# Performance work log

Measured on AMD Instinct MI355X. Metric: run time of the kernel, lower is better.

Reference implementation:

```python
import jax, jax.numpy as jnp
import numpy as np

B, L, ENC_IN, C_OUT = 4, 2048, 64, 64
D_MODEL, N_HEADS, D_FF, E_LAYERS = 1024, 16, 4096, 4
CA_K = 5  # ChannelAttention1D kernel: int(|log2(1024)+1|/2)=5 (odd)


def _layer_norm(x, w, b, eps=1e-5):
    m = x.mean(-1, keepdims=True)
    v = ((x - m) ** 2).mean(-1, keepdims=True)
    return (x - m) * jax.lax.rsqrt(v + eps) * w + b


def _flow_attention(q, k, v):
    # q,k,v: [B, L, H, D] -> work in [B, H, L, D]
    q = jax.nn.sigmoid(jnp.swapaxes(q, 1, 2))
    k = jax.nn.sigmoid(jnp.swapaxes(k, 1, 2))
    v = jnp.swapaxes(v, 1, 2)
    eps = 1e-6
    Lq = q.shape[2]
    S = k.shape[2]
    nr = 1.0 / jnp.einsum('bhld,bhd->bhl', q + eps, k.sum(axis=2) + eps)
    nc = 1.0 / jnp.einsum('bhsd,bhd->bhs', k + eps, q.sum(axis=2) + eps)
    nrr = jnp.einsum('bhld,bhd->bhl', q + eps, (k * nc[..., None]).sum(axis=2) + eps)
    ncr = jnp.einsum('bhsd,bhd->bhs', k + eps, (q * nr[..., None]).sum(axis=2) + eps)
    nrr = jax.nn.sigmoid(nrr * (float(Lq) / float(S)))
    ncr = jax.nn.softmax(ncr, axis=-1) * S
    kv = jnp.einsum('bhsd,bhse->bhde', k, v * ncr[..., None])  # [B,H,D,Dv]
    out = jnp.einsum('bhld,bhde->bhle', q, kv) * nr[..., None] * nrr[..., None]
    return jnp.swapaxes(out, 1, 2)  # [B, L, H, Dv]


def _token_embed(x, w):
    # x: [B, L, Cin]; circular conv1d kernel=3, pad=1, no bias
    xt = jnp.swapaxes(x, 1, 2)  # [B, Cin, L]
    xt = jnp.concatenate([xt[..., -1:], xt, xt[..., :1]], axis=-1)
    y = jax.lax.conv_general_dilated(xt, w, (1,), 'VALID',
                                     dimension_numbers=('NCH', 'OIH', 'NCH'))
    return jnp.swapaxes(y, 1, 2)  # [B, L, d_model]


def _channel_att(x, w):
    # x: [B, L, C]; squeeze over L, conv over channel axis, sigmoid gate
    y = x.mean(axis=1, keepdims=True)  # [B, 1, C]
    pad = CA_K // 2
    yp = jnp.pad(y, ((0, 0), (0, 0), (pad, pad)))
    yc = jax.lax.conv_general_dilated(yp, w.reshape(1, 1, CA_K), (1,), 'VALID',
                                      dimension_numbers=('NCH', 'OIH', 'NCH'))
    return x * jax.nn.sigmoid(yc)


def _encoder_layer(x, Wq, bq, Wk, bk, Wv, bv, Wo, bo,
                   ln1w, ln1b, ln2w, ln2b, c1w, c1b, c2w, c2b):
    Bx, Lx, _ = x.shape
    q = (x @ Wq.T + bq).reshape(Bx, Lx, N_HEADS, -1)
    k = (x @ Wk.T + bk).reshape(Bx, Lx, N_HEADS, -1)
    v = (x @ Wv.T + bv).reshape(Bx, Lx, N_HEADS, -1)
    a = _flow_attention(q, k, v).reshape(Bx, Lx, -1)
    a = a @ Wo.T + bo
    x = _layer_norm(x + a, ln1w, ln1b)
    y = jax.nn.relu(jnp.einsum('bld,fd->blf', x, c1w) + c1b)  # conv1 k=1
    y = jnp.einsum('blf,df->bld', y, c2w) + c2b               # conv2 k=1
    return _layer_norm(x + y, ln2w, ln2b)


def setup_inputs() -> dict:
    key = jax.random.key(0)
    ks = jax.random.split(key, 16)
    s = 0.02
    E, D, F = E_LAYERS, D_MODEL, D_FF
    inp = {
        'x': jax.random.normal(ks[0], (B, L, ENC_IN), jnp.float32),
        'tok_conv_w': jax.random.normal(ks[1], (D, ENC_IN, 3), jnp.float32) * s,
        'Wq': jax.random.normal(ks[2], (E, D, D), jnp.float32) * s,
        'bq': jnp.zeros((E, D), jnp.float32),
        'Wk': jax.random.normal(ks[3], (E, D, D), jnp.float32) * s,
        'bk': jnp.zeros((E, D), jnp.float32),
        'Wv': jax.random.normal(ks[4], (E, D, D), jnp.float32) * s,
        'bv': jnp.zeros((E, D), jnp.float32),
        'Wo': jax.random.normal(ks[5], (E, D, D), jnp.float32) * s,
        'bo': jnp.zeros((E, D), jnp.float32),
        'conv1_w': jax.random.normal(ks[6], (E, F, D), jnp.float32) * s,
        'conv1_b': jnp.zeros((E, F), jnp.float32),
        'conv2_w': jax.random.normal(ks[7], (E, D, F), jnp.float32) * s,
        'conv2_b': jnp.zeros((E, D), jnp.float32),
        'ln1_w': jnp.ones((E, D), jnp.float32),
        'ln1_b': jnp.zeros((E, D), jnp.float32),
        'ln2_w': jnp.ones((E, D), jnp.float32),
        'ln2_b': jnp.zeros((E, D), jnp.float32),
        'ca_w': jax.random.normal(ks[8], (E, CA_K), jnp.float32) * 0.2,
        'lnf_w': jnp.ones((D,), jnp.float32),
        'lnf_b': jnp.zeros((D,), jnp.float32),
        'proj_w': jax.random.normal(ks[9], (C_OUT, D), jnp.float32) * s,
        'proj_b': jnp.zeros((C_OUT,), jnp.float32),
    }
    return inp


def reference(x, tok_conv_w, Wq, bq, Wk, bk, Wv, bv, Wo, bo,
              conv1_w, conv1_b, conv2_w, conv2_b,
              ln1_w, ln1_b, ln2_w, ln2_b, ca_w,
              lnf_w, lnf_b, proj_w, proj_b):
    h = _token_embed(x, tok_conv_w)  # dropout = identity (eval)
    for i in range(E_LAYERS):
        h = _encoder_layer(h, Wq[i], bq[i], Wk[i], bk[i], Wv[i], bv[i], Wo[i], bo[i],
                           ln1_w[i], ln1_b[i], ln2_w[i], ln2_b[i],
                           conv1_w[i], conv1_b[i], conv2_w[i], conv2_b[i])
        h = _channel_att(h, ca_w[i])
    # Encoder re-applies the last attention layer after the conv loop (faithful)
    i = E_LAYERS - 1
    h = _encoder_layer(h, Wq[i], bq[i], Wk[i], bk[i], Wv[i], bv[i], Wo[i], bo[i],
                       ln1_w[i], ln1_b[i], ln2_w[i], ln2_b[i],
                       conv1_w[i], conv1_b[i], conv2_w[i], conv2_b[i])
    h = _layer_norm(h, lnf_w, lnf_b)
    return h @ proj_w.T + proj_b
```

## Files before the change

### kernel.cpp

```cpp
#include <hip/hip_runtime.h>
#include <stdint.h>

#define L_SEQ 2048
#define DM 1024
#define NH 16
#define DFF 4096
#define NB 4
#define ROWS (NB * L_SEQ)

typedef __attribute__((ext_vector_type(8))) __bf16 bf16x8;
typedef __attribute__((ext_vector_type(4))) float f32x4;

__device__ __forceinline__ float bf2f(unsigned short u) {
  union { unsigned int i; float f; } x; x.i = ((unsigned int)u) << 16; return x.f;
}
__device__ __forceinline__ unsigned short f2bf(float f) {
  union { float f; unsigned int i; } x; x.f = f;
  unsigned int r = x.i + 0x7FFFu + ((x.i >> 16) & 1u);
  return (unsigned short)(r >> 16);
}

typedef __attribute__((address_space(3))) void lds_void;
typedef const __attribute__((address_space(1))) void gbl_void;

__device__ __forceinline__ void stage16(const void* g, void* ldsbase) {
  __builtin_amdgcn_global_load_lds((gbl_void*)g, (lds_void*)ldsbase, 16, 0, 0);
}

#define MFMA1(d, a, b) (d) = __builtin_amdgcn_mfma_f32_16x16x32_bf16((a), (b), (d), 0, 0, 0)

__global__ __launch_bounds__(256, 4)
void gemm_f(const unsigned short* __restrict__ A,
            const unsigned short* __restrict__ B,
            const float* __restrict__ bias,
            unsigned short* __restrict__ C16,
            float* __restrict__ C32,
            int K, int lda, int ldc, int n_limit, int act)
{
  __shared__ __attribute__((aligned(16))) unsigned short sm[16384];
  char* smb = (char*)sm;
  const int tid  = threadIdx.x;
  const int wave = tid >> 6, lane = tid & 63;
  const int l16 = lane & 15, quad = lane >> 4;
  const int lb = lane << 4;
  const int wm = wave >> 1, wn = wave & 1;

  const int bx = (int)blockIdx.x, by = (int)blockIdx.y;

  const unsigned short* Ab = A + (size_t)bx * 128 * lda;
  const unsigned short* Bb = B + (size_t)by * 128 * K;

  const int rb0 = ((wave >> 1) << 4) + l16;
  const int cb0 = ((wave & 1) << 5) + (quad << 3);

  f32x4 acc[4][4] = {};
  const int T = K >> 6;

  for (int t = 0; t < T; ++t) {
    const unsigned short* sa = Ab + (size_t)rb0 * lda + t * 64 + cb0;
    const unsigned short* sb = Bb + (size_t)rb0 * K   + t * 64 + cb0;
    char* da = smb + wave * 1024;
    char* db = smb + 16384 + wave * 1024;
#pragma unroll
    for (int j = 0; j < 4; ++j) {
      stage16(sa + (size_t)(j * 32) * lda, da + j * 4096);
      stage16(sb + (size_t)(j * 32) * K,   db + j * 4096);
    }
    __syncthreads();
#pragma unroll
    for (int ks = 0; ks < 2; ++ks) {
      bf16x8 af[4], bf[4];
#pragma unroll
      for (int i = 0; i < 4; ++i) {
        af[i] = *(const bf16x8*)(smb + ((((wm * 4 + i) * 2 + ks)) << 10) + lb);
        bf[i] = *(const bf16x8*)(smb + 16384 + ((((wn * 4 + i) * 2 + ks)) << 10) + lb);
      }
#pragma unroll
      for (int i = 0; i < 4; ++i)
#pragma unroll
        for (int j = 0; j < 4; ++j)
          MFMA1(acc[i][j], af[i], bf[j]);
    }
    __syncthreads();
  }

  const int row0 = bx * 128 + wm * 64 + quad * 4;
  const int col0 = by * 128 + wn * 64 + l16;
#pragma unroll
  for (int nj = 0; nj < 4; ++nj) {
    const int col = col0 + nj * 16;
    if (col >= n_limit) continue;
    const float bv = bias ? bias[col] : 0.0f;
    const bool sig = (act == 2) || (act == 3 && col < 2048);
#pragma unroll
    for (int mi = 0; mi < 4; ++mi) {
#pragma unroll
      for (int r = 0; r < 4; ++r) {
        const int row = row0 + mi * 16 + r;
        float v = acc[mi][nj][r] + bv;
        if (act == 1) v = fmaxf(v, 0.0f);
        else if (sig) v = 1.0f / (1.0f + __expf(-v));
        if (C32) C32[(size_t)row * ldc + col] = v;
        if (C16) C16[(size_t)row * ldc + col] = f2bf(v);
      }
    }
  }
}


__global__ __launch_bounds__(256)
void fa_sums(const unsigned short* __restrict__ Q, const unsigned short* __restrict__ K,
             int ld, float* __restrict__ ksp, float* __restrict__ qsp)
{
  const int bh = blockIdx.x, chunk = blockIdx.y;
  const size_t base = ((size_t)(bh >> 4) * L_SEQ) * ld + (size_t)(bh & 15) * 64;
  const int t = threadIdx.x, lane = t & 63, wave = t >> 6;
  __shared__ float red[256];
  float ks = 0.f, qs = 0.f;
  const int l0 = chunk * 256 + wave * 64;
  for (int i = 0; i < 64; i++) {
    const size_t idx = base + (size_t)(l0 + i) * ld + lane;
    ks += bf2f(K[idx]);
    qs += bf2f(Q[idx]);
  }
  red[t] = ks; __syncthreads();
  if (t < 64) ksp[(bh * 8 + chunk) * 64 + t] = red[t] + red[t + 64] + red[t + 128] + red[t + 192];
  __syncthreads();
  red[t] = qs; __syncthreads();
  if (t < 64) qsp[(bh * 8 + chunk) * 64 + t] = red[t] + red[t + 64] + red[t + 128] + red[t + 192];
}

__global__ __launch_bounds__(256)
void fa_rows1(const unsigned short* __restrict__ Q, const unsigned short* __restrict__ K,
              int ld, const float* __restrict__ ksp, const float* __restrict__ qsp,
              float* __restrict__ nr, float* __restrict__ t1p, float* __restrict__ t2p)
{
  const int bh = blockIdx.x, chunk = blockIdx.y;
  const size_t base = ((size_t)(bh >> 4) * L_SEQ) * ld + (size_t)(bh & 15) * 64;
  const int t = threadIdx.x, lane = t & 63, wave = t >> 6;
  const float eps = 1e-6f;
  __shared__ float s_kse[64], s_qse[64], red[256];
  if (t < 64) {
    float s = 0.f;
    for (int j = 0; j < 8; j++) s += ksp[(bh * 8 + j) * 64 + t];
    s_kse[t] = s + eps;
  } else if (t < 128) {
    const int d = t - 64;
    float s = 0.f;
    for (int j = 0; j < 8; j++) s += qsp[(bh * 8 + j) * 64 + d];
    s_qse[d] = s + eps;
  }
  __syncthreads();
  const float kse = s_kse[lane], qse = s_qse[lane];
  float t1a = 0.f, t2a = 0.f;
  for (int i = 0; i < 32; i++) {
    const int l = chunk * 128 + wave + 4 * i;
    const size_t idx = base + (size_t)l * ld + lane;
    const float q = bf2f(Q[idx]), k = bf2f(K[idx]);
    float a = (q + eps) * kse;
    float c = (k + eps) * qse;
#pragma unroll
    for (int off = 32; off; off >>= 1) { a += __shfl_xor(a, off); c += __shfl_xor(c, off); }
    const float nrl = 1.f / a, ncl = 1.f / c;
    if (lane == 0) nr[bh * L_SEQ + l] = nrl;
    t1a += k * ncl;
    t2a += q * nrl;
  }
  red[t] = t1a; __syncthreads();
  if (t < 64) t1p[(bh * 16 + chunk) * 64 + t] = red[t] + red[t + 64] + red[t + 128] + red[t + 192];
  __syncthreads();
  red[t] = t2a; __syncthreads();
  if (t < 64) t2p[(bh * 16 + chunk) * 64 + t] = red[t] + red[t + 64] + red[t + 128] + red[t + 192];
}

__global__ __launch_bounds__(256)
void fa_rows2(const unsigned short* __restrict__ Q, const unsigned short* __restrict__ K,
              int ld, const float* __restrict__ t1p, const float* __restrict__ t2p,
              float* __restrict__ nr, float* __restrict__ sc)
{
  const int bh = blockIdx.x, chunk = blockIdx.y;
  const size_t base = ((size_t)(bh >> 4) * L_SEQ) * ld + (size_t)(bh & 15) * 64;
  const int t = threadIdx.x, lane = t & 63, wave = t >> 6;
  const float eps = 1e-6f;
  __shared__ float s_t1e[64], s_t2e[64];
  if (t < 64) {
    float s = 0.f;
    for (int j = 0; j < 16; j++) s += t1p[(bh * 16 + j) * 64 + t];
    s_t1e[t] = s + eps;
  } else if (t < 128) {
    const int d = t - 64;
    float s = 0.f;
    for (int j = 0; j < 16; j++) s += t2p[(bh * 16 + j) * 64 + d];
    s_t2e[d] = s + eps;
  }
  __syncthreads();
  const float t1e = s_t1e[lane], t2e = s_t2e[lane];
  for (int i = 0; i < 32; i++) {
    const int l = chunk * 128 + wave + 4 * i;
    const size_t idx = base + (size_t)l * ld + lane;
    const float q = bf2f(Q[idx]), k = bf2f(K[idx]);
    float a = (q + eps) * t1e;
    float c = (k + eps) * t2e;
#pragma unroll
    for (int off = 32; off; off >>= 1) { a += __shfl_xor(a, off); c += __shfl_xor(c, off); }
    if (lane == 0) {
      nr[bh * L_SEQ + l] *= 1.f / (1.f + __expf(-a));
      sc[bh * L_SEQ + l] = c;
    }
  }
}

__global__ __launch_bounds__(256)
void fa_softmax(float* __restrict__ sc, float* __restrict__ kv)
{
  const int bh = blockIdx.x, t = threadIdx.x;
  __shared__ float red[256];
  float4* kvz = (float4*)(kv + bh * 64 * 64);
  for (int j = 0; j < 4; j++) kvz[t + 256 * j] = make_float4(0.f, 0.f, 0.f, 0.f);

  float* row = sc + bh * L_SEQ;
  float m = -3.4e38f;
  for (int l = t; l < L_SEQ; l += 256) m = fmaxf(m, row[l]);
  red[t] = m; __syncthreads();
  for (int s = 128; s > 0; s >>= 1) { if (t < s) red[t] = fmaxf(red[t], red[t + s]); __syncthreads(); }
  const float mx = red[0];
  __syncthreads();
  float ps = 0.f;
  float pv[8];
#pragma unroll
  for (int j = 0; j < 8; j++) {
    const int l = t + 256 * j;
    pv[j] = __expf(row[l] - mx);
    ps += pv[j];
  }
  red[t] = ps; __syncthreads();
  for (int s = 128; s > 0; s >>= 1) { if (t < s) red[t] += red[t + s]; __syncthreads(); }
  const float scale = (float)L_SEQ / red[0];
#pragma unroll
  for (int j = 0; j < 8; j++) row[t + 256 * j] = pv[j] * scale;
}

__global__ __launch_bounds__(256)
void fa_kv(const unsigned short* __restrict__ K, const unsigned short* __restrict__ V,
           int ld, const float* __restrict__ sc, float* __restrict__ kv)
{
  const int bh = blockIdx.x, chunk = blockIdx.y;
  const size_t base = ((size_t)(bh >> 4) * L_SEQ) * ld + (size_t)(bh & 15) * 64;
  const int t = threadIdx.x, lane = t & 63, wave = t >> 6;
  const int l16 = lane & 15, quad = lane >> 4;
  __shared__ __attribute__((aligned(16))) unsigned short s_kT[64 * 72];
  __shared__ __attribute__((aligned(16))) unsigned short s_vT[64 * 72];

  f32x4 acc5[4] = {};
  for (int sub = 0; sub < 2; sub++) {
    const int l0 = chunk * 128 + sub * 64;
#pragma unroll
    for (int it = 0; it < 4; it++) {
      const int task = it * 256 + t;
      const int l = task >> 4;
      const int g = task & 15;
      const size_t gidx = base + (size_t)(l0 + l) * ld + g * 4;
      const ushort4 k4 = *(const ushort4*)(K + gidx);
      const ushort4 v4 = *(const ushort4*)(V + gidx);
      const float wgt = sc[bh * L_SEQ + l0 + l];
      s_kT[(g * 4 + 0) * 72 + l] = k4.x;
      s_kT[(g * 4 + 1) * 72 + l] = k4.y;
      s_kT[(g * 4 + 2) * 72 + l] = k4.z;
      s_kT[(g * 4 + 3) * 72 + l] = k4.w;
      s_vT[(g * 4 + 0) * 72 + l] = f2bf(bf2f(v4.x) * wgt);
      s_vT[(g * 4 + 1) * 72 + l] = f2bf(bf2f(v4.y) * wgt);
      s_vT[(g * 4 + 2) * 72 + l] = f2bf(bf2f(v4.z) * wgt);
      s_vT[(g * 4 + 3) * 72 + l] = f2bf(bf2f(v4.w) * wgt);
    }
    __syncthreads();
#pragma unroll
    for (int ks = 0; ks < 2; ks++) {
      const bf16x8 af = *(const bf16x8*)&s_kT[(wave * 16 + l16) * 72 + ks * 32 + quad * 8];
#pragma unroll
      for (int et = 0; et < 4; et++) {
        const bf16x8 bf = *(const bf16x8*)&s_vT[(et * 16 + l16) * 72 + ks * 32 + quad * 8];
        acc5[et] = __builtin_amdgcn_mfma_f32_16x16x32_bf16(af, bf, acc5[et], 0, 0, 0);
      }
    }
    __syncthreads();
  }
#pragma unroll
  for (int et = 0; et < 4; et++)
#pragma unroll
    for (int r = 0; r < 4; r++)
      atomicAdd(&kv[bh * 4096 + (wave * 16 + quad * 4 + r) * 64 + et * 16 + l16], acc5[et][r]);
}

__global__ __launch_bounds__(256)
void fa_out(const unsigned short* __restrict__ Q, int ld, const float* __restrict__ kv,
            const float* __restrict__ nr, unsigned short* O)
{
  const int bh = blockIdx.x, chunk = blockIdx.y;
  const size_t base = ((size_t)(bh >> 4) * L_SEQ) * ld + (size_t)(bh & 15) * 64;
  const int t = threadIdx.x, lane = t & 63, wave = t >> 6;
  const int l16 = lane & 15, quad = lane >> 4;
  __shared__ __attribute__((aligned(16))) unsigned short s_kvT[64 * 72];

#pragma unroll
  for (int j = 0; j < 16; j++) {
    const int i = t + 256 * j;
    const int d = i >> 6, e = i & 63;
    s_kvT[e * 72 + d] = f2bf(kv[bh * 4096 + i]);
  }
  __syncthreads();

  bf16x8 bfr6[4][2];
#pragma unroll
  for (int et = 0; et < 4; et++)
#pragma unroll
    for (int ks = 0; ks < 2; ks++)
      bfr6[et][ks] = *(const bf16x8*)&s_kvT[(et * 16 + l16) * 72 + ks * 32 + quad * 8];

#pragma unroll
  for (int ti = 0; ti < 2; ti++) {
    const int l0 = chunk * 128 + (wave * 2 + ti) * 16;
    f32x4 oc[4] = {};
#pragma unroll
    for (int ks = 0; ks < 2; ks++) {
      const bf16x8 aq = *(const bf16x8*)(Q + base + (size_t)(l0 + l16) * ld + ks * 32 + quad * 8);
#pragma unroll
      for (int et = 0; et < 4; et++)
        oc[et] = __builtin_amdgcn_mfma_f32_16x16x32_bf16(aq, bfr6[et][ks], oc[et], 0, 0, 0);
    }
#pragma unroll
    for (int r = 0; r < 4; r++) {
      const int l = l0 + quad * 4 + r;
      const float scl = nr[bh * L_SEQ + l];
#pragma unroll
      for (int et = 0; et < 4; et++)
        O[base + (size_t)l * ld + et * 16 + l16] = f2bf(oc[et][r] * scl);
    }
  }
}

__global__ __launch_bounds__(256)
void ln_fused(const float* res, const float* __restrict__ add,
              const float* __restrict__ w, const float* __restrict__ bb,
              float* out32, unsigned short* out16)
{
  const int row = blockIdx.x * 4 + (threadIdx.x >> 6);
  const int lane = threadIdx.x & 63;
  const size_t roff = (size_t)row * DM;
  const float4* rp = (const float4*)(res + roff);
  const float4* ap = add ? (const float4*)(add + roff) : nullptr;

  float x[16], s = 0.f, s2 = 0.f;
#pragma unroll
  for (int q4 = 0; q4 < 4; q4++) {
    float4 v = rp[lane * 4 + q4];
    if (ap) { float4 a = ap[lane * 4 + q4]; v.x += a.x; v.y += a.y; v.z += a.z; v.w += a.w; }
    x[q4 * 4 + 0] = v.x; x[q4 * 4 + 1] = v.y; x[q4 * 4 + 2] = v.z; x[q4 * 4 + 3] = v.w;
    s += v.x + v.y + v.z + v.w;
    s2 += v.x * v.x + v.y * v.y + v.z * v.z + v.w * v.w;
  }
#pragma unroll
  for (int off = 32; off; off >>= 1) { s += __shfl_xor(s, off); s2 += __shfl_xor(s2, off); }
  const float mean = s * (1.f / DM);
  const float var = s2 * (1.f / DM) - mean * mean;
  const float rstd = rsqrtf(var + 1e-5f);
#pragma unroll
  for (int j = 0; j < 16; j++) {
    const int c = lane * 16 + j;
    x[j] = (x[j] - mean) * rstd * w[c] + bb[c];
  }
  if (out32) {
    float4* op = (float4*)(out32 + roff);
#pragma unroll
    for (int q4 = 0; q4 < 4; q4++) {
      float4 v; v.x = x[q4*4+0]; v.y = x[q4*4+1]; v.z = x[q4*4+2]; v.w = x[q4*4+3];
      op[lane * 4 + q4] = v;
    }
  }
  if (out16) {
#pragma unroll
    for (int q4 = 0; q4 < 4; q4++) {
      ushort4 u;
      u.x = f2bf(x[q4*4+0]); u.y = f2bf(x[q4*4+1]); u.z = f2bf(x[q4*4+2]); u.w = f2bf(x[q4*4+3]);
      *(ushort4*)(out16 + roff + lane * 16 + q4 * 4) = u;
    }
  }
}

__global__ void ca_zero(float* __restrict__ ybar) {
  const int i = blockIdx.x * 256 + threadIdx.x;
  if (i < NB * DM) ybar[i] = 0.f;
}
__global__ void ca_mean(const unsigned short* __restrict__ H16, float* __restrict__ ybar) {
  const int b = blockIdx.x, cc = blockIdx.y, lc = blockIdx.z;
  const int c = cc * 256 + threadIdx.x;
  float s = 0.f;
  for (int l = lc * 256; l < lc * 256 + 256; l++)
    s += bf2f(H16[((size_t)(b * L_SEQ + l)) * DM + c]);
  atomicAdd(&ybar[b * DM + c], s);
}
__global__ void ca_gate(const float* __restrict__ ybar, const float* __restrict__ cw,
                        float* __restrict__ gate) {
  const int i = blockIdx.x * 256 + threadIdx.x;
  if (i >= NB * DM) return;
  const int b = i >> 10, c = i & 1023;
  float acc = 0.f;
#pragma unroll
  for (int j = 0; j < 5; j++) {
    const int cc = c + j - 2;
    const float yv = (cc >= 0 && cc < DM) ? ybar[b * DM + cc] * (1.f / L_SEQ) : 0.f;
    acc += cw[j] * yv;
  }
  gate[i] = 1.f / (1.f + __expf(-acc));
}
__global__ void ca_apply(float* __restrict__ H32, unsigned short* __restrict__ H16,
                         const float* __restrict__ gate) {
  const size_t i = ((size_t)blockIdx.x * 256 + threadIdx.x) * 4;
  const int row = (int)(i >> 10);
  const int b = row >> 11;
  const int c = (int)(i & 1023);
  float4 v = *(float4*)(H32 + i);
  v.x *= gate[b * DM + c + 0];
  v.y *= gate[b * DM + c + 1];
  v.z *= gate[b * DM + c + 2];
  v.w *= gate[b * DM + c + 3];
  *(float4*)(H32 + i) = v;
  unsigned short* hp = H16 + i;
  hp[0] = f2bf(v.x); hp[1] = f2bf(v.y); hp[2] = f2bf(v.z); hp[3] = f2bf(v.w);
}

__global__ void embed_gather(const float* __restrict__ x, unsigned short* __restrict__ Ae) {
  const int i = blockIdx.x * 256 + threadIdx.x;
  if (i >= ROWS * 192) return;
  const int row = i / 192, kk = i % 192;
  const int t3 = kk >> 6, c = kk & 63;
  const int b = row >> 11, l = row & 2047;
  const int ls = (l + t3 - 1 + L_SEQ) & 2047;
  Ae[i] = f2bf(x[((size_t)(b * L_SEQ + ls)) * 64 + c]);
}
__global__ void embed_repack(const float* __restrict__ w, unsigned short* __restrict__ We) {
  const int i = blockIdx.x * 256 + threadIdx.x;
  if (i >= DM * 192) return;
  const int f = i / 192, kk = i % 192;
  const int t3 = kk >> 6, c = kk & 63;
  We[i] = f2bf(w[(f * 64 + c) * 3 + t3]);
}
__global__ void pad_proj(const float* __restrict__ pw, unsigned short* __restrict__ Wp) {
  const int i = blockIdx.x * 256 + threadIdx.x;
  if (i >= 128 * DM) return;
  Wp[i] = ((i >> 10) < 64) ? f2bf(pw[i]) : (unsigned short)0;
}
__global__ void pack_qkv_bias(const float* __restrict__ bq, const float* __restrict__ bk,
                              const float* __restrict__ bv, float* __restrict__ bqkv) {
  const int i = blockIdx.x * 256 + threadIdx.x;
  if (i >= 3072) return;
  bqkv[i] = (i < 1024) ? bq[i] : (i < 2048 ? bk[i - 1024] : bv[i - 2048]);
}
__global__ void cvt_layer_weights(const float* __restrict__ Wq, const float* __restrict__ Wk,
                                  const float* __restrict__ Wv, const float* __restrict__ Wo,
                                  const float* __restrict__ c1, const float* __restrict__ c2,
                                  unsigned short* __restrict__ Wl, unsigned short* __restrict__ WlFF) {
  const int g = blockIdx.x * 256 + threadIdx.x;
  const int i = g << 2;
  const float* src; unsigned short* dst;
  if (i < (1 << 22)) {
    const int w = i >> 20, off = i & ((1 << 20) - 1);
    const float* srcs[4] = {Wq, Wk, Wv, Wo};
    src = srcs[w] + off; dst = Wl + (w << 20) + off;
  } else {
    const int j = i - (1 << 22);
    const int w = j >> 22, off = j & ((1 << 22) - 1);
    src = (w ? c2 : c1) + off; dst = WlFF + (w << 22) + off;
  }
  const float4 v = *(const float4*)src;
  ushort4 u; u.x = f2bf(v.x); u.y = f2bf(v.y); u.z = f2bf(v.z); u.w = f2bf(v.w);
  *(ushort4*)dst = u;
}

extern "C" void kernel_launch(void* const* d_in, const int* in_sizes, int n_in,
                              void* d_out, int out_size, void* d_ws, size_t ws_size,
                              hipStream_t stream) {
  const float* x     = (const float*)d_in[0];
  const float* tokw  = (const float*)d_in[1];
  const float* Wq    = (const float*)d_in[2];
  const float* bq    = (const float*)d_in[3];
  const float* Wk    = (const float*)d_in[4];
  const float* bk    = (const float*)d_in[5];
  const float* Wv    = (const float*)d_in[6];
  const float* bv    = (const float*)d_in[7];
  const float* Wo    = (const float*)d_in[8];
  const float* bo    = (const float*)d_in[9];
  const float* c1w   = (const float*)d_in[10];
  const float* c1b   = (const float*)d_in[11];
  const float* c2w   = (const float*)d_in[12];
  const float* c2b   = (const float*)d_in[13];
  const float* ln1w  = (const float*)d_in[14];
  const float* ln1b  = (const float*)d_in[15];
  const float* ln2w  = (const float*)d_in[16];
  const float* ln2b  = (const float*)d_in[17];
  const float* caw   = (const float*)d_in[18];
  const float* lnfw  = (const float*)d_in[19];
  const float* lnfb  = (const float*)d_in[20];
  const float* projw = (const float*)d_in[21];
  const float* projb = (const float*)d_in[22];

  char* ws = (char*)d_ws;
  float*          R32 = (float*)(ws);
  unsigned short* R16 = (unsigned short*)(ws + ((size_t)32 << 20));
  float*          A32 = (float*)(ws + ((size_t)48 << 20));
  unsigned short* U   = (unsigned short*)(ws + ((size_t)80 << 20));
  unsigned short* QKV16 = U;
  unsigned short* F16   = U;
  char* fa = ws + ((size_t)128 << 20);
  float* fa_nr  = (float*)(fa);
  float* fa_sc  = (float*)(fa + (512 << 10));
  float* fa_ksp = (float*)(fa + (1024 << 10));
  float* fa_qsp = (float*)(fa + (1152 << 10));
  float* fa_t1p = (float*)(fa + (1280 << 10));
  float* fa_t2p = (float*)(fa + (1792 << 10));
  float* fa_kvb = (float*)(fa + (2304 << 10));
  unsigned short* Wl   = (unsigned short*)(ws + ((size_t)144 << 20));
  unsigned short* WlFF = (unsigned short*)(ws + ((size_t)152 << 20));
  char* misc = ws + ((size_t)168 << 20);
  float*          ybar = (float*)misc;
  float*          gate = (float*)(misc + (16 << 10));
  float*          bqkv = (float*)(misc + (32 << 10));
  unsigned short* We   = (unsigned short*)(misc + (64 << 10));
  unsigned short* Wp   = (unsigned short*)(misc + (512 << 10));

  const int BIG = 1 << 30;
  auto gemm = [&](const unsigned short* A, const unsigned short* B, const float* bias,
                  unsigned short* C16, float* C32, int N, int K, int lda, int ldc,
                  int nlim, int act) {
    dim3 grid(ROWS / 128, N / 128);
    gemm_f<<<grid, dim3(256), 0, stream>>>(A, B, bias, C16, C32, K, lda, ldc, nlim, act);
  };

  embed_gather<<<(ROWS * 192 + 255) / 256, 256, 0, stream>>>(x, U);
  embed_repack<<<(DM * 192 + 255) / 256, 256, 0, stream>>>(tokw, We);
  gemm(U, We, nullptr, R16, R32, DM, 192, 192, DM, BIG, 0);

  for (int it = 0; it < 5; it++) {
    const int i = (it < 4) ? it : 3;
    if (it != 4) {
      cvt_layer_weights<<<(3 << 20) / 256, 256, 0, stream>>>(
          Wq + ((size_t)i << 20), Wk + ((size_t)i << 20),
          Wv + ((size_t)i << 20), Wo + ((size_t)i << 20),
          c1w + ((size_t)i << 22), c2w + ((size_t)i << 22), Wl, WlFF);
      pack_qkv_bias<<<12, 256, 0, stream>>>(bq + i * DM, bk + i * DM, bv + i * DM, bqkv);
    }
    const unsigned short* Wo16 = Wl + (3 << 20);
    const unsigned short* C116 = WlFF;
    const unsigned short* C216 = WlFF + (1 << 22);

    gemm(R16, Wl, bqkv, QKV16, nullptr, 3072, DM, DM, 3072, BIG, 3);

    const unsigned short* Qp = QKV16;
    const unsigned short* Kp = QKV16 + 1024;
    unsigned short*       Vp = QKV16 + 2048;

    fa_sums   <<<dim3(64, 8),  256, 0, stream>>>(Qp, Kp, 3072, fa_ksp, fa_qsp);
    fa_rows1  <<<dim3(64, 16), 256, 0, stream>>>(Qp, Kp, 3072, fa_ksp, fa_qsp, fa_nr, fa_t1p, fa_t2p);
    fa_rows2  <<<dim3(64, 16), 256, 0, stream>>>(Qp, Kp, 3072, fa_t1p, fa_t2p, fa_nr, fa_sc);
    fa_softmax<<<dim3(64),     256, 0, stream>>>(fa_sc, fa_kvb);
    fa_kv     <<<dim3(64, 16), 256, 0, stream>>>(Kp, Vp, 3072, fa_sc, fa_kvb);
    fa_out    <<<dim3(64, 16), 256, 0, stream>>>(Qp, 3072, fa_kvb, fa_nr, Vp);

    gemm(Vp, Wo16, bo + i * DM, nullptr, A32, DM, DM, 3072, DM, BIG, 0);
    ln_fused<<<ROWS / 4, 256, 0, stream>>>(R32, A32, ln1w + i * DM, ln1b + i * DM, R32, R16);
    gemm(R16, C116, c1b + i * DFF, F16, nullptr, DFF, DM, DM, DFF, BIG, 1);
    gemm(F16, C216, c2b + i * DM, nullptr, A32, DM, DFF, DFF, DM, BIG, 0);
    ln_fused<<<ROWS / 4, 256, 0, stream>>>(R32, A32, ln2w + i * DM, ln2b + i * DM, R32, R16);

    if (it < 4) {
      ca_zero<<<16, 256, 0, stream>>>(ybar);
      ca_mean<<<dim3(NB, 4, 8), 256, 0, stream>>>(R16, ybar);
      ca_gate<<<16, 256, 0, stream>>>(ybar, caw + i * 5, gate);
      ca_apply<<<(ROWS * DM / 4) / 256, 256, 0, stream>>>(R32, R16, gate);
    }
  }

  ln_fused<<<ROWS / 4, 256, 0, stream>>>(R32, nullptr, lnfw, lnfb, nullptr, U);
  pad_proj<<<(128 * DM + 255) / 256, 256, 0, stream>>>(projw, Wp);
  gemm(U, Wp, projb, nullptr, (float*)d_out, 128, DM, DM, 64, 64, 0);

  (void)in_sizes; (void)n_in; (void)out_size; (void)ws_size;
}
```

Before: 3.234 ms.

## Halve GEMM K-tile to 32 and stage bf16 output through LDS for vector stores

The GEMM kernel now stages a 32-wide K slice per iteration instead of 64, halving shared memory to 16 KB and dropping the occupancy hint from launch_bounds. The bf16 output path writes results into LDS in two 64-row passes and then emits coalesced 16-byte global stores instead of scattered 2-byte stores. This aims to cut store transaction count and possibly raise occupancy. In exchange there are twice as many barriers per K, and the bf16 path ignores n_limit.

```diff
diff --git a/kernel.cpp b/kernel.cpp
--- a/kernel.cpp
+++ b/kernel.cpp
@@ -29,15 +29,15 @@
 
 #define MFMA1(d, a, b) (d) = __builtin_amdgcn_mfma_f32_16x16x32_bf16((a), (b), (d), 0, 0, 0)
 
-__global__ __launch_bounds__(256, 4)
-void gemm_f(const unsigned short* __restrict__ A,
-            const unsigned short* __restrict__ B,
-            const float* __restrict__ bias,
-            unsigned short* __restrict__ C16,
-            float* __restrict__ C32,
-            int K, int lda, int ldc, int n_limit, int act)
-{
-  __shared__ __attribute__((aligned(16))) unsigned short sm[16384];
+__global__ __launch_bounds__(256)
+void gemm_bt(const unsigned short* __restrict__ A,
+             const unsigned short* __restrict__ B,
+             const float* __restrict__ bias,
+             unsigned short* __restrict__ C16,
+             float* __restrict__ C32,
+             int K, int lda, int ldc, int n_limit, int act)
+{
+  __shared__ __attribute__((aligned(16))) unsigned short sm[8192];
   char* smb = (char*)sm;
   const int tid  = threadIdx.x;
   const int wave = tid >> 6, lane = tid & 63;
@@ -50,59 +50,89 @@
   const unsigned short* Ab = A + (size_t)bx * 128 * lda;
   const unsigned short* Bb = B + (size_t)by * 128 * K;
 
-  const int rb0 = ((wave >> 1) << 4) + l16;
-  const int cb0 = ((wave & 1) << 5) + (quad << 3);
-
   f32x4 acc[4][4] = {};
-  const int T = K >> 6;
-
-  for (int t = 0; t < T; ++t) {
-    const unsigned short* sa = Ab + (size_t)rb0 * lda + t * 64 + cb0;
-    const unsigned short* sb = Bb + (size_t)rb0 * K   + t * 64 + cb0;
-    char* da = smb + wave * 1024;
-    char* db = smb + 16384 + wave * 1024;
-#pragma unroll
-    for (int j = 0; j < 4; ++j) {
-      stage16(sa + (size_t)(j * 32) * lda, da + j * 4096);
-      stage16(sb + (size_t)(j * 32) * K,   db + j * 4096);
-    }
+
+  for (int k0 = 0; k0 < K; k0 += 32) {
+    const unsigned short* sa = Ab + (size_t)(wave * 16 + l16) * lda + k0 + quad * 8;
+    const unsigned short* sb = Bb + (size_t)(wave * 16 + l16) * K   + k0 + quad * 8;
+    stage16(sa,                      smb + wave * 1024);
+    stage16(sa + (size_t)64 * lda,   smb + (wave + 4) * 1024);
+    stage16(sb,                      smb + 8192 + wave * 1024);
+    stage16(sb + (size_t)64 * K,     smb + 8192 + (wave + 4) * 1024);
     __syncthreads();
-#pragma unroll
-    for (int ks = 0; ks < 2; ++ks) {
-      bf16x8 af[4], bf[4];
-#pragma unroll
-      for (int i = 0; i < 4; ++i) {
-        af[i] = *(const bf16x8*)(smb + ((((wm * 4 + i) * 2 + ks)) << 10) + lb);
-        bf[i] = *(const bf16x8*)(smb + 16384 + ((((wn * 4 + i) * 2 + ks)) << 10) + lb);
-      }
-#pragma unroll
-      for (int i = 0; i < 4; ++i)
-#pragma unroll
-        for (int j = 0; j < 4; ++j)
-          MFMA1(acc[i][j], af[i], bf[j]);
-    }
+
+    bf16x8 af[4], bf[4];
+#pragma unroll
+    for (int i = 0; i < 4; ++i) {
+      af[i] = *(const bf16x8*)(smb + (wm * 4 + i) * 1024 + lb);
+      bf[i] = *(const bf16x8*)(smb + 8192 + (wn * 4 + i) * 1024 + lb);
+    }
+#pragma unroll
+    for (int i = 0; i < 4; ++i)
+#pragma unroll
+      for (int j = 0; j < 4; ++j)
+        MFMA1(acc[i][j], af[i], bf[j]);
     __syncthreads();
   }
 
   const int row0 = bx * 128 + wm * 64 + quad * 4;
   const int col0 = by * 128 + wn * 64 + l16;
-#pragma unroll
-  for (int nj = 0; nj < 4; ++nj) {
-    const int col = col0 + nj * 16;
-    if (col >= n_limit) continue;
-    const float bv = bias ? bias[col] : 0.0f;
-    const bool sig = (act == 2) || (act == 3 && col < 2048);
-#pragma unroll
-    for (int mi = 0; mi < 4; ++mi) {
-#pragma unroll
-      for (int r = 0; r < 4; ++r) {
-        const int row = row0 + mi * 16 + r;
-        float v = acc[mi][nj][r] + bv;
-        if (act == 1) v = fmaxf(v, 0.0f);
-        else if (sig) v = 1.0f / (1.0f + __expf(-v));
-        if (C32) C32[(size_t)row * ldc + col] = v;
-        if (C16) C16[(size_t)row * ldc + col] = f2bf(v);
+
+  if (C32) {
+#pragma unroll
+    for (int nj = 0; nj < 4; ++nj) {
+      const int col = col0 + nj * 16;
+      if (col >= n_limit) continue;
+      const float bv = bias ? bias[col] : 0.0f;
+      const bool sig = (act == 2) || (act == 3 && col < 2048);
+#pragma unroll
+      for (int mi = 0; mi < 4; ++mi) {
+#pragma unroll
+        for (int r = 0; r < 4; ++r) {
+          const int row = row0 + mi * 16 + r;
+          float v = acc[mi][nj][r] + bv;
+          if (act == 1) v = fmaxf(v, 0.0f);
+          else if (sig) v = 1.0f / (1.0f + __expf(-v));
+          C32[(size_t)row * ldc + col] = v;
+        }
       }
+    }
+  }
+
+  if (C16) {
+    unsigned short* s_c = sm;
+#pragma unroll
+    for (int p = 0; p < 2; ++p) {
+      if (wm == p) {
+#pragma unroll
+        for (int nj = 0; nj < 4; ++nj) {
+          const int col = col0 + nj * 16;
+          const float bv = bias ? bias[col] : 0.0f;
+          const bool sig = (act == 2) || (act == 3 && col < 2048);
+          const int lcol = wn * 64 + nj * 16 + l16;
+#pragma unroll
+          for (int mi = 0; mi < 4; ++mi) {
+#pragma unroll
+            for (int r = 0; r < 4; ++r) {
+              float v = acc[mi][nj][r] + bv;
+              if (act == 1) v = fmaxf(v, 0.0f);
+              else if (sig) v = 1.0f / (1.0f + __expf(-v));
+              s_c[(mi * 16 + quad * 4 + r) * 128 + lcol] = f2bf(v);
+            }
+          }
+        }
+      }
+      __syncthreads();
+      const int rowg0 = bx * 128 + p * 64;
+#pragma unroll
+      for (int j = 0; j < 4; ++j) {
+        const int c = j * 256 + tid;
+        const int lr = c >> 4;
+        const int off = (c & 15) * 8;
+        *(uint4*)(C16 + (size_t)(rowg0 + lr) * ldc + by * 128 + off) =
+            *(const uint4*)&s_c[lr * 128 + off];
+      }
+      __syncthreads();
     }
   }
 }
@@ -532,7 +562,7 @@
                   unsigned short* C16, float* C32, int N, int K, int lda, int ldc,
                   int nlim, int act) {
     dim3 grid(ROWS / 128, N / 128);
-    gemm_f<<<grid, dim3(256), 0, stream>>>(A, B, bias, C16, C32, K, lda, ldc, nlim, act);
+    gemm_bt<<<grid, dim3(256), 0, stream>>>(A, B, bias, C16, C32, K, lda, ldc, nlim, act);
   };
 
   embed_gather<<<(ROWS * 192 + 255) / 256, 256, 0, stream>>>(x, U);
```

Result: slower. 3.411 ms (+5.5%).
